# Kernel tuning notes

Measured on AMD Instinct MI355X. Metric: run time of the kernel, lower is better.

Reference implementation:

```python
import jax, jax.numpy as jnp
import numpy as np

HIDDEN = 4096
NUM_HEADS = 32
NUM_KV_HEADS = 8
HEAD_DIM = HIDDEN // NUM_HEADS  # 128
GROUPS = NUM_HEADS // NUM_KV_HEADS  # 4
ROPE_THETA = 10000.0


def setup_inputs() -> dict:
    key = jax.random.key(0)
    k0, k1, k2, k3, k4 = jax.random.split(key, 5)
    b, s = 2, 2048
    hidden_states = jax.random.normal(k0, (b, s, HIDDEN), dtype=jnp.float32)
    position_ids = jnp.broadcast_to(jnp.arange(s, dtype=jnp.int64), (b, s))
    sc = 1.0 / np.sqrt(HIDDEN)
    Wq = jax.random.normal(k1, (HIDDEN, NUM_HEADS * HEAD_DIM), dtype=jnp.float32) * sc
    Wk = jax.random.normal(k2, (HIDDEN, NUM_KV_HEADS * HEAD_DIM), dtype=jnp.float32) * sc
    Wv = jax.random.normal(k3, (HIDDEN, NUM_KV_HEADS * HEAD_DIM), dtype=jnp.float32) * sc
    Wo = jax.random.normal(k4, (NUM_HEADS * HEAD_DIM, HIDDEN), dtype=jnp.float32) * sc
    return {"hidden_states": hidden_states, "position_ids": position_ids,
            "Wq": Wq, "Wk": Wk, "Wv": Wv, "Wo": Wo}


def _rope(x, cos, sin):
    # x: [b, s, h, d]; cos/sin: [b, s, 1, d]
    d2 = x.shape[-1] // 2
    x1, x2 = x[..., :d2], x[..., d2:]
    rot = jnp.concatenate([-x2, x1], axis=-1)
    return x * cos + rot * sin


def reference(hidden_states, position_ids, Wq, Wk, Wv, Wo):
    b, s, _ = hidden_states.shape
    scale = 1.0 / np.sqrt(HEAD_DIM)
    # projections (Linear, no bias) kept in [b, s, h, d] layout
    q = (hidden_states @ Wq).reshape(b, s, NUM_HEADS, HEAD_DIM)
    k = (hidden_states @ Wk).reshape(b, s, NUM_KV_HEADS, HEAD_DIM)
    v = (hidden_states @ Wv).reshape(b, s, NUM_KV_HEADS, HEAD_DIM)
    # RoPE: emb = cat(freqs, freqs)
    inv_freq = 1.0 / (ROPE_THETA ** (jnp.arange(0, HEAD_DIM, 2, dtype=jnp.float32) / HEAD_DIM))
    freqs = position_ids.astype(jnp.float32)[..., None] * inv_freq  # [b, s, d/2]
    emb = jnp.concatenate([freqs, freqs], axis=-1)[:, :, None, :]   # [b, s, 1, d]
    cos, sin = jnp.cos(emb), jnp.sin(emb)
    q = _rope(q, cos, sin)
    k = _rope(k, cos, sin)
    # GQA: query head h maps to kv head h // GROUPS (repeat_kv is contiguous expand)
    qg = q.reshape(b, s, NUM_KV_HEADS, GROUPS, HEAD_DIM)
    scores = jnp.einsum('bqkgd,bskd->bkgqs', qg, k) * scale  # [b, kv, g, s_q, s_k]
    probs = jax.nn.softmax(scores, axis=-1)
    out = jnp.einsum('bkgqs,bskd->bqkgd', probs, v).reshape(b, s, HIDDEN)
    return out @ Wo
```

## Files before the change

### kernel.cpp

```cpp
#include <hip/hip_runtime.h>

typedef unsigned short u16;
typedef unsigned int u32;
typedef __attribute__((ext_vector_type(8))) __bf16 bf16x8;
typedef __attribute__((ext_vector_type(4))) float f32x4;

__device__ __forceinline__ u16 f2bf(float f) {
  union { float f; u32 u; } v; v.f = f;
  u32 r = v.u + 0x7fffu + ((v.u >> 16) & 1u);
  return (u16)(r >> 16);
}
__device__ __forceinline__ float bf2f(u16 h) {
  return __uint_as_float(((u32)h) << 16);
}
__device__ __forceinline__ void gld16(void* lds, const void* g) {
  __builtin_amdgcn_global_load_lds(
      (__attribute__((address_space(1))) void*)g,
      (__attribute__((address_space(3))) void*)lds, 16, 0, 0);
}

__global__ void convert_x(const float* __restrict__ src, u16* __restrict__ dst) {
  const size_t c = (size_t)blockIdx.x * blockDim.x + threadIdx.x;
  const float* s = src + c * 8;
  u16 t[8];
#pragma unroll
  for (int i = 0; i < 8; ++i) t[i] = f2bf(s[i]);
  ((uint4*)dst)[c] = *(const uint4*)t;
}

__global__ void transpose_w(const float* __restrict__ srcf, u16* __restrict__ dst,
                            int K, int N) {
  __shared__ u16 tile[64][72];
  const int r0 = blockIdx.y * 64, c0 = blockIdx.x * 64;
  const int tr = threadIdx.x >> 2;
  const int tc = (threadIdx.x & 3) * 16;
  const float* src = srcf + (size_t)(r0 + tr) * N + c0 + tc;
  u16* t = &tile[tr][tc];
#pragma unroll
  for (int i = 0; i < 16; ++i) t[i] = f2bf(src[i]);
  __syncthreads();
  u16 tmp[16];
#pragma unroll
  for (int i = 0; i < 16; ++i) tmp[i] = tile[tc + i][tr];
  uint4* gd = (uint4*)(dst + (size_t)(c0 + tr) * K + r0 + tc);
  gd[0] = *(uint4*)&tmp[0];
  gd[1] = *(uint4*)&tmp[8];
}

__global__ void transpose_v(const u16* __restrict__ V, u16* __restrict__ Vt) {
  __shared__ u16 tile[64][72];
  const int z = blockIdx.z, b = z >> 3, h = z & 7;
  const int s0 = blockIdx.y * 64;
  const int d0 = blockIdx.x * 64;
  const u16* src = V + ((size_t)(b * 2048 + s0)) * 1024 + h * 128 + d0;
  u16* dst = Vt + ((size_t)((b * 8 + h) * 128 + d0)) * 2048 + s0;
  const int tr = threadIdx.x >> 2;
  const int tc = (threadIdx.x & 3) * 16;
  const uint4* gs = (const uint4*)(src + (size_t)tr * 1024 + tc);
  *(uint4*)&tile[tr][tc] = gs[0];
  *(uint4*)&tile[tr][tc + 8] = gs[1];
  __syncthreads();
  u16 tmp[16];
#pragma unroll
  for (int i = 0; i < 16; ++i) tmp[i] = tile[tc + i][tr];
  uint4* gd = (uint4*)(dst + (size_t)tr * 2048 + tc);
  gd[0] = *(uint4*)&tmp[0];
  gd[1] = *(uint4*)&tmp[8];
}

template <int OUT32>
__global__ __launch_bounds__(256, 2) void gemm_bt128(
    const u16* __restrict__ A, const u16* __restrict__ Bt,
    void* __restrict__ Cv, int K, int N) {
  __shared__ u16 As[128 * 64];
  __shared__ u16 Bs[128 * 64];
  const int tid = threadIdx.x;
  const int wave = tid >> 6, lane = tid & 63;
  const int m0 = blockIdx.y * 128, n0 = blockIdx.x * 128;
  const int wr = (wave >> 1) * 64, wc = (wave & 1) * 64;
  const int lrow = lane & 15, quad = lane >> 4;
  const int cbase = wave * 64 + lane;

  f32x4 acc[4][4];
#pragma unroll
  for (int i = 0; i < 4; ++i)
#pragma unroll
    for (int j = 0; j < 4; ++j) acc[i][j] = (f32x4){0.f, 0.f, 0.f, 0.f};

  for (int k0 = 0; k0 < K; k0 += 64) {
#pragma unroll
    for (int r = 0; r < 4; ++r) {
      const int c = r * 256 + cbase;
      const int row = c >> 3, col = (c & 7) * 8;
      gld16(&As[(size_t)(r * 4 + wave) * 512],
            A + (size_t)(m0 + row) * K + k0 + col);
      gld16(&Bs[(size_t)(r * 4 + wave) * 512],
            Bt + (size_t)(n0 + row) * K + k0 + col);
    }
    __syncthreads();
#pragma unroll
    for (int kk = 0; kk < 2; ++kk) {
      const int ko = kk * 32 + quad * 8;
      bf16x8 af[4], bfr[4];
#pragma unroll
      for (int i = 0; i < 4; ++i)
        af[i] = *(const bf16x8*)&As[(wr + i * 16 + lrow) * 64 + ko];
#pragma unroll
      for (int j = 0; j < 4; ++j)
        bfr[j] = *(const bf16x8*)&Bs[(wc + j * 16 + lrow) * 64 + ko];
#pragma unroll
      for (int i = 0; i < 4; ++i)
#pragma unroll
        for (int j = 0; j < 4; ++j)
          acc[i][j] = __builtin_amdgcn_mfma_f32_16x16x32_bf16(af[i], bfr[j], acc[i][j], 0, 0, 0);
    }
    __syncthreads();
  }
#pragma unroll
  for (int i = 0; i < 4; ++i)
#pragma unroll
    for (int j = 0; j < 4; ++j)
#pragma unroll
      for (int reg = 0; reg < 4; ++reg) {
        const int row = m0 + wr + i * 16 + quad * 4 + reg;
        const int col = n0 + wc + j * 16 + lrow;
        if (OUT32)
          ((float*)Cv)[(size_t)row * N + col] = acc[i][j][reg];
        else
          ((u16*)Cv)[(size_t)row * N + col] = f2bf(acc[i][j][reg]);
      }
}

__global__ void rope_kernel(u16* __restrict__ Q, u16* __restrict__ Kc) {
  const int row = blockIdx.x;
  const float p = (float)(row & 2047);
  const float csc = 0.088388347762774597f * 1.4426950408889634f;
  for (int t = threadIdx.x; t < 2560; t += 256) {
    u16* base;
    int d;
    float sc;
    if (t < 2048) { const int h = t >> 6; d = t & 63; base = Q + (size_t)row * 4096 + h * 128; sc = csc; }
    else { const int tt = t - 2048; const int h = tt >> 6; d = tt & 63; base = Kc + (size_t)row * 1024 + h * 128; sc = 1.f; }
    const float inv = exp2f((float)d * -0.20762050593046807f);
    const float f = p * inv;
    float s, c;
    sincosf(f, &s, &c);
    const float x1 = bf2f(base[d]);
    const float x2 = bf2f(base[d + 64]);
    base[d] = f2bf((x1 * c - x2 * s) * sc);
    base[d + 64] = f2bf((x2 * c + x1 * s) * sc);
  }
}

__global__ __launch_bounds__(256, 1) void attn(
    const u16* __restrict__ Q, const u16* __restrict__ Kc,
    const u16* __restrict__ Vt, u16* __restrict__ O) {
  __shared__ u16 smem[25600];
  u16* Qs = smem;
  u16* Ks = smem;
  u16* Vs = smem + 8192;
  u16* Ps = smem + 16384;
  const int tid = threadIdx.x, wave = tid >> 6, lane = tid & 63;
  const int qt = blockIdx.x, qh = blockIdx.y, b = blockIdx.z;
  const int kvh = qh >> 2;
  const int lrow = lane & 15, quad = lane >> 4;
  const int swz = (lrow & 7) << 3;

  const u16* qb = Q + ((size_t)(b * 2048 + qt * 128)) * 4096 + qh * 128;
#pragma unroll
  for (int r = 0; r < 8; ++r) {
    const int c = (r * 4 + wave) * 64 + lane;
    const int row = c >> 4, scol = (c & 15) ^ (row & 7);
    gld16(&Qs[(size_t)(r * 4 + wave) * 512],
          qb + (size_t)row * 4096 + scol * 8);
  }
  __syncthreads();
  bf16x8 aq[2][4];
#pragma unroll
  for (int i = 0; i < 2; ++i)
#pragma unroll
    for (int kk = 0; kk < 4; ++kk)
      aq[i][kk] = *(const bf16x8*)
          &Qs[(wave * 32 + i * 16 + lrow) * 128 + ((kk * 32 + quad * 8) ^ swz)];
  __syncthreads();

  {
    const u16* kb = Kc + ((size_t)(b * 2048)) * 1024 + kvh * 128;
#pragma unroll
    for (int r = 0; r < 4; ++r) {
      const int c = (r * 4 + wave) * 64 + lane;
      const int row = c >> 4, scol = (c & 15) ^ (row & 7);
      gld16(&Ks[(size_t)(r * 4 + wave) * 512],
            kb + (size_t)row * 1024 + scol * 8);
    }
  }
  __syncthreads();

  f32x4 acco[2][8];
#pragma unroll
  for (int i = 0; i < 2; ++i)
#pragma unroll
    for (int j = 0; j < 8; ++j) acco[i][j] = (f32x4){0.f, 0.f, 0.f, 0.f};
  float m_i[2], l_i[2];
#pragma unroll
  for (int i = 0; i < 2; ++i) { m_i[i] = -INFINITY; l_i[i] = 0.f; }

  const u16* vbase = Vt + ((size_t)((b * 8 + kvh) * 128)) * 2048;

  for (int kv0 = 0; kv0 < 2048; kv0 += 64) {
#pragma unroll
    for (int r = 0; r < 4; ++r) {
      const int c = (r * 4 + wave) * 64 + lane;
      const int row = c >> 3, scol = (c & 7) ^ (row & 7);
      gld16(&Vs[(size_t)(r * 4 + wave) * 512],
            vbase + (size_t)row * 2048 + kv0 + scol * 8);
    }

    f32x4 s[2][4];
#pragma unroll
    for (int i = 0; i < 2; ++i)
#pragma unroll
      for (int j = 0; j < 4; ++j) s[i][j] = (f32x4){0.f, 0.f, 0.f, 0.f};
    __builtin_amdgcn_s_setprio(1);
#pragma unroll
    for (int kk = 0; kk < 4; ++kk) {
      const int ko = (kk * 32 + quad * 8) ^ swz;
#pragma unroll
      for (int j = 0; j < 4; ++j) {
        const bf16x8 bk = *(const bf16x8*)&Ks[(j * 16 + lrow) * 128 + ko];
        s[0][j] = __builtin_amdgcn_mfma_f32_16x16x32_bf16(bk, aq[0][kk], s[0][j], 0, 0, 0);
        s[1][j] = __builtin_amdgcn_mfma_f32_16x16x32_bf16(bk, aq[1][kk], s[1][j], 0, 0, 0);
      }
    }
    __builtin_amdgcn_s_setprio(0);

#pragma unroll
    for (int i = 0; i < 2; ++i) {
      float mx = s[i][0][0];
#pragma unroll
      for (int j = 0; j < 4; ++j)
#pragma unroll
        for (int reg = 0; reg < 4; ++reg) mx = fmaxf(mx, s[i][j][reg]);
      mx = fmaxf(mx, __shfl_xor(mx, 16));
      mx = fmaxf(mx, __shfl_xor(mx, 32));
      const bool grow = !__all(mx <= m_i[i] + 8.f);
      float mnew = m_i[i], al = 1.f;
      if (grow) {
        mnew = fmaxf(m_i[i], mx);
        al = exp2f(m_i[i] - mnew);
        m_i[i] = mnew;
      }
      float rs = 0.f;
#pragma unroll
      for (int j = 0; j < 4; ++j)
#pragma unroll
        for (int reg = 0; reg < 4; ++reg) {
          const float p0 = exp2f(s[i][j][reg] - mnew);
          s[i][j][reg] = p0;
          rs += p0;
        }
      rs += __shfl_xor(rs, 16);
      rs += __shfl_xor(rs, 32);
      l_i[i] = l_i[i] * al + rs;
      if (grow) {
#pragma unroll
        for (int j = 0; j < 8; ++j)
#pragma unroll
          for (int reg = 0; reg < 4; ++reg) acco[i][j][reg] *= al;
      }
    }

#pragma unroll
    for (int i = 0; i < 2; ++i)
#pragma unroll
      for (int j = 0; j < 4; ++j) {
        u16 t4[4];
#pragma unroll
        for (int reg = 0; reg < 4; ++reg) t4[reg] = f2bf(s[i][j][reg]);
        *(uint2*)&Ps[(wave * 32 + i * 16 + lrow) * 72 + j * 16 + quad * 4] =
            *(const uint2*)t4;
      }
    __syncthreads();

    if (kv0 + 64 < 2048) {
      const u16* kb = Kc + ((size_t)(b * 2048 + kv0 + 64)) * 1024 + kvh * 128;
#pragma unroll
      for (int r = 0; r < 4; ++r) {
        const int c = (r * 4 + wave) * 64 + lane;
        const int row = c >> 4, scol = (c & 15) ^ (row & 7);
        gld16(&Ks[(size_t)(r * 4 + wave) * 512],
              kb + (size_t)row * 1024 + scol * 8);
      }
    }

    __builtin_amdgcn_s_setprio(1);
#pragma unroll
    for (int kk = 0; kk < 2; ++kk) {
      const int ko = kk * 32 + quad * 8;
      const int kov = ko ^ swz;
      const bf16x8 ap0 = *(const bf16x8*)&Ps[(wave * 32 + lrow) * 72 + ko];
      const bf16x8 ap1 = *(const bf16x8*)&Ps[(wave * 32 + 16 + lrow) * 72 + ko];
#pragma unroll
      for (int j = 0; j < 8; ++j) {
        const bf16x8 bv = *(const bf16x8*)&Vs[(j * 16 + lrow) * 64 + kov];
        acco[0][j] = __builtin_amdgcn_mfma_f32_16x16x32_bf16(bv, ap0, acco[0][j], 0, 0, 0);
        acco[1][j] = __builtin_amdgcn_mfma_f32_16x16x32_bf16(bv, ap1, acco[1][j], 0, 0, 0);
      }
    }
    __builtin_amdgcn_s_setprio(0);
    __syncthreads();
  }

#pragma unroll
  for (int i = 0; i < 2; ++i) {
    const float inv = 1.0f / l_i[i];
    const int row = b * 2048 + qt * 128 + wave * 32 + i * 16 + lrow;
#pragma unroll
    for (int j = 0; j < 8; ++j) {
      u16 t4[4];
#pragma unroll
      for (int reg = 0; reg < 4; ++reg) t4[reg] = f2bf(acco[i][j][reg] * inv);
      *(uint2*)&O[(size_t)row * 4096 + qh * 128 + j * 16 + quad * 4] =
          *(const uint2*)t4;
    }
  }
}

extern "C" void kernel_launch(void* const* d_in, const int* in_sizes, int n_in,
                              void* d_out, int out_size, void* d_ws, size_t ws_size,
                              hipStream_t stream) {
  const float* X  = (const float*)d_in[0];
  const float* Wq = (const float*)d_in[2];
  const float* Wk = (const float*)d_in[3];
  const float* Wv = (const float*)d_in[4];
  const float* Wo = (const float*)d_in[5];
  u16* ws = (u16*)d_ws;

  u16* Xb = ws;
  u16* R0 = Xb + 16777216;
  u16* R1 = R0 + 16777216;
  u16* R2 = R1 + 16777216;
  u16* R3 = R2 + 4194304;
  u16* R4 = R3 + 4194304;
  u16* Qb = R1, *Kb = R3, *Vb = R4, *Vt = R2, *Ob = R0, *WoT = R1;

  convert_x<<<8192, 256, 0, stream>>>(X, Xb);

  transpose_w<<<dim3(64, 64), 256, 0, stream>>>(Wq, R0, 4096, 4096);
  gemm_bt128<0><<<dim3(32, 32), 256, 0, stream>>>(Xb, R0, Qb, 4096, 4096);

  transpose_w<<<dim3(16, 64), 256, 0, stream>>>(Wk, R0, 4096, 1024);
  gemm_bt128<0><<<dim3(8, 32), 256, 0, stream>>>(Xb, R0, Kb, 4096, 1024);

  transpose_w<<<dim3(16, 64), 256, 0, stream>>>(Wv, R0, 4096, 1024);
  gemm_bt128<0><<<dim3(8, 32), 256, 0, stream>>>(Xb, R0, Vb, 4096, 1024);

  rope_kernel<<<4096, 256, 0, stream>>>(Qb, Kb);
  transpose_v<<<dim3(2, 32, 16), 256, 0, stream>>>(Vb, Vt);

  attn<<<dim3(16, 32, 2), 256, 0, stream>>>(Qb, Kb, Vt, Ob);

  transpose_w<<<dim3(64, 64), 256, 0, stream>>>(Wo, WoT, 4096, 4096);
  gemm_bt128<1><<<dim3(32, 32), 256, 0, stream>>>(Ob, WoT, d_out, 4096, 4096);
}
```

Baseline: 1.083 ms.

## Keep softmax probabilities in registers by permuting K rows, dropping the P LDS round-trip

```diff
diff --git a/kernel.cpp b/kernel.cpp
--- a/kernel.cpp
+++ b/kernel.cpp
@@ -4,6 +4,7 @@
 typedef unsigned int u32;
 typedef __attribute__((ext_vector_type(8))) __bf16 bf16x8;
 typedef __attribute__((ext_vector_type(4))) float f32x4;
+typedef __attribute__((ext_vector_type(4))) u32 u32x4;
 
 __device__ __forceinline__ u16 f2bf(float f) {
   union { float f; u32 u; } v; v.f = f;
@@ -12,6 +13,9 @@
 }
 __device__ __forceinline__ float bf2f(u16 h) {
   return __uint_as_float(((u32)h) << 16);
+}
+__device__ __forceinline__ u32 pk2(float a, float b) {
+  return (u32)f2bf(a) | ((u32)f2bf(b) << 16);
 }
 __device__ __forceinline__ void gld16(void* lds, const void* g) {
   __builtin_amdgcn_global_load_lds(
@@ -152,14 +156,13 @@
   }
 }
 
-__global__ __launch_bounds__(256, 1) void attn(
+__global__ __launch_bounds__(256, 3) void attn(
     const u16* __restrict__ Q, const u16* __restrict__ Kc,
     const u16* __restrict__ Vt, u16* __restrict__ O) {
-  __shared__ u16 smem[25600];
+  __shared__ u16 smem[16384];
   u16* Qs = smem;
   u16* Ks = smem;
   u16* Vs = smem + 8192;
-  u16* Ps = smem + 16384;
   const int tid = threadIdx.x, wave = tid >> 6, lane = tid & 63;
   const int qt = blockIdx.x, qh = blockIdx.y, b = blockIdx.z;
   const int kvh = qh >> 2;
@@ -189,9 +192,11 @@
 #pragma unroll
     for (int r = 0; r < 4; ++r) {
       const int c = (r * 4 + wave) * 64 + lane;
-      const int row = c >> 4, scol = (c & 15) ^ (row & 7);
+      const int m = c >> 4, scol = (c & 15) ^ (m & 7);
+      const int srcrow = ((m >> 5) << 5) | (((m >> 2) & 3) << 3) |
+                         (((m >> 4) & 1) << 2) | (m & 3);
       gld16(&Ks[(size_t)(r * 4 + wave) * 512],
-            kb + (size_t)row * 1024 + scol * 8);
+            kb + (size_t)srcrow * 1024 + scol * 8);
     }
   }
   __syncthreads();
@@ -270,15 +275,15 @@
       }
     }
 
+    u32x4 pw[2][2];
 #pragma unroll
     for (int i = 0; i < 2; ++i)
 #pragma unroll
-      for (int j = 0; j < 4; ++j) {
-        u16 t4[4];
-#pragma unroll
-        for (int reg = 0; reg < 4; ++reg) t4[reg] = f2bf(s[i][j][reg]);
-        *(uint2*)&Ps[(wave * 32 + i * 16 + lrow) * 72 + j * 16 + quad * 4] =
-            *(const uint2*)t4;
+      for (int kk = 0; kk < 2; ++kk) {
+        pw[i][kk].x = pk2(s[i][2 * kk][0], s[i][2 * kk][1]);
+        pw[i][kk].y = pk2(s[i][2 * kk][2], s[i][2 * kk][3]);
+        pw[i][kk].z = pk2(s[i][2 * kk + 1][0], s[i][2 * kk + 1][1]);
+        pw[i][kk].w = pk2(s[i][2 * kk + 1][2], s[i][2 * kk + 1][3]);
       }
     __syncthreads();
 
@@ -287,19 +292,20 @@
 #pragma unroll
       for (int r = 0; r < 4; ++r) {
         const int c = (r * 4 + wave) * 64 + lane;
-        const int row = c >> 4, scol = (c & 15) ^ (row & 7);
+        const int m = c >> 4, scol = (c & 15) ^ (m & 7);
+        const int srcrow = ((m >> 5) << 5) | (((m >> 2) & 3) << 3) |
+                           (((m >> 4) & 1) << 2) | (m & 3);
         gld16(&Ks[(size_t)(r * 4 + wave) * 512],
-              kb + (size_t)row * 1024 + scol * 8);
+              kb + (size_t)srcrow * 1024 + scol * 8);
       }
     }
 
     __builtin_amdgcn_s_setprio(1);
 #pragma unroll
     for (int kk = 0; kk < 2; ++kk) {
-      const int ko = kk * 32 + quad * 8;
-      const int kov = ko ^ swz;
-      const bf16x8 ap0 = *(const bf16x8*)&Ps[(wave * 32 + lrow) * 72 + ko];
-      const bf16x8 ap1 = *(const bf16x8*)&Ps[(wave * 32 + 16 + lrow) * 72 + ko];
+      const int kov = (kk * 32 + quad * 8) ^ swz;
+      const bf16x8 ap0 = __builtin_bit_cast(bf16x8, pw[0][kk]);
+      const bf16x8 ap1 = __builtin_bit_cast(bf16x8, pw[1][kk]);
 #pragma unroll
       for (int j = 0; j < 8; ++j) {
         const bf16x8 bv = *(const bf16x8*)&Vs[(j * 16 + lrow) * 64 + kov];
```

Result: no change. 1.065 ms (-1.7%).
